# Kernel tuning notes

Hardware: AMD Instinct MI355X
Metric: run time of the kernel (lower is better)

The kernel has to match this reference:

```python
import jax, jax.numpy as jnp
import numpy as np

M, N, D = 4, 65536, 256

def setup_inputs() -> dict:
    key = jax.random.key(0)
    k1, k2, k3 = jax.random.split(key, 3)
    x = jax.random.normal(k1, (M, N, D), dtype=jnp.float32)
    # W[i,j] is the (out,in) weight of fusion_layers[i][j]; b[i,j] its bias.
    W = jax.random.normal(k2, (M, M, D, D), dtype=jnp.float32) * (1.0 / np.sqrt(D))
    b = jax.random.normal(k3, (M, M, D), dtype=jnp.float32) * 0.02
    return {"x": x, "W": W, "b": b}

def reference(x, W, b):
    # x: [M, N, D] stacked modality features (zip(*features) rows vectorized over N)
    # out[i] = x[i] + sum_{j != i} (x[j] @ W[i,j]^T + b[i,j])
    m = x.shape[0]
    mask = (1.0 - jnp.eye(m)).astype(x.dtype)            # zero on diagonal (skip i==j)
    y = jnp.einsum('ijef,jnf->ijne', W, x) + b[:, :, None, :]  # [M, M, N, D]
    out = x + jnp.einsum('ij,ijne->ine', mask, y)         # fused masked accumulation
    return out
```

## Files before the change

### kernel.cpp

```cpp
#include <hip/hip_runtime.h>
#include <hip/hip_bf16.h>
#include <stdint.h>

#define NN 65536
#define DD 256

typedef uint32_t u32;
typedef __attribute__((ext_vector_type(4))) float f32x4;
typedef __attribute__((ext_vector_type(4))) u32 u32x4;
typedef __attribute__((ext_vector_type(2))) u32 u32x2;
typedef __attribute__((ext_vector_type(8))) short s16x8;

__device__ inline unsigned short f2bf(float f) {
    union { float f; u32 u; } v; v.f = f;
    u32 u = v.u;
    return (unsigned short)((u + 0x7fffu + ((u >> 16) & 1u)) >> 16);
}

__device__ inline void gl2lds16(const void* g, void* s) {
    __builtin_amdgcn_global_load_lds(
        (const __attribute__((address_space(1))) void*)g,
        (__attribute__((address_space(3))) void*)s, 16, 0, 0);
}

__global__ void prep_w256(const float* __restrict__ W, unsigned short* __restrict__ Wimg) {
    int t = blockIdx.x * blockDim.x + threadIdx.x;
    int E = t * 4;
    int tile = E >> 14;
    int pin = E & 16383;
    int col = pin >> 6;
    int r2e = pin & 63;
    int ct = tile >> 4;
    int j = (tile >> 2) & 3;
    int kk = tile & 3;
    int kl = r2e ^ ((col & 7) << 3);
    int i = ct;
    int e = col;
    int f = kk * 64 + kl;
    u32 p0, p1;
    if (i == j) {
        unsigned short d0 = (e == f + 0) ? 0x3F80 : 0;
        unsigned short d1 = (e == f + 1) ? 0x3F80 : 0;
        unsigned short d2 = (e == f + 2) ? 0x3F80 : 0;
        unsigned short d3 = (e == f + 3) ? 0x3F80 : 0;
        p0 = (u32)d0 | ((u32)d1 << 16);
        p1 = (u32)d2 | ((u32)d3 << 16);
    } else {
        f32x4 w = *(const f32x4*)(W + ((size_t)((i * 4 + j) * 256 + e) << 8) + f);
        p0 = (u32)f2bf(w[0]) | ((u32)f2bf(w[1]) << 16);
        p1 = (u32)f2bf(w[2]) | ((u32)f2bf(w[3]) << 16);
    }
    u32x2 pr = {p0, p1};
    *(u32x2*)(Wimg + E) = pr;
}

__global__ void prep_w128(const float* __restrict__ W, unsigned short* __restrict__ Wimg) {
    int t = blockIdx.x * blockDim.x + threadIdx.x;
    int E = t * 4;
    int tile = E >> 13;
    int pin = E & 8191;
    int col = pin >> 6;
    int r2e = pin & 63;
    int ct = tile >> 4;
    int j = (tile >> 2) & 3;
    int kk = tile & 3;
    int kl = r2e ^ ((col & 7) << 3);
    int c = ct * 128 + col;
    int i = c >> 8, e = c & 255;
    int f = kk * 64 + kl;
    u32 p0, p1;
    if (i == j) {
        p0 = 0u; p1 = 0u;
    } else {
        f32x4 w = *(const f32x4*)(W + ((size_t)((i * 4 + j) * 256 + e) << 8) + f);
        p0 = (u32)f2bf(w[0]) | ((u32)f2bf(w[1]) << 16);
        p1 = (u32)f2bf(w[2]) | ((u32)f2bf(w[3]) << 16);
    }
    u32x2 pr = {p0, p1};
    *(u32x2*)(Wimg + E) = pr;
}

__global__ void prep_x(const float* __restrict__ x, unsigned short* __restrict__ Ximg) {
    int t = blockIdx.x * blockDim.x + threadIdx.x;
    long long E = (long long)t * 4;
    int tile = (int)(E >> 14);
    int pin = (int)(E & 16383);
    int row = pin >> 6;
    int r2e = pin & 63;
    int kk = tile & 3;
    int rt = (tile >> 2) & 255;
    int j = tile >> 10;
    int kl = r2e ^ ((row & 7) << 3);
    int n = rt * 256 + row;
    int f = kk * 64 + kl;
    f32x4 v = *(const f32x4*)(x + ((size_t)j * NN + n) * DD + f);
    u32 p0 = (u32)f2bf(v[0]) | ((u32)f2bf(v[1]) << 16);
    u32 p1 = (u32)f2bf(v[2]) | ((u32)f2bf(v[3]) << 16);
    u32x2 pr = {p0, p1};
    *(u32x2*)(Ximg + E) = pr;
}

__global__ void prep_b(const float* __restrict__ b, float* __restrict__ bsum) {
    int c = blockIdx.x * blockDim.x + threadIdx.x;
    if (c >= 1024) return;
    int i = c >> 8, e = c & 255;
    float s = 0.0f;
    #pragma unroll
    for (int j = 0; j < 4; ++j)
        if (j != i) s += b[((i * 4 + j) << 8) + e];
    bsum[c] = s;
}

__global__ __launch_bounds__(512, 2) void fusion_gemm4(
    const unsigned short* __restrict__ Wimg, const unsigned short* __restrict__ Ximg,
    const float* __restrict__ bsum, float* __restrict__ out) {
    __shared__ __attribute__((aligned(16))) char lds[2][65536];

    const int tid = threadIdx.x;
    const int bid = blockIdx.x;
    const int xcd = bid & 7;
    const int slot = bid >> 3;
    const int ct = slot & 3;
    const int rhi = slot >> 2;
    const int rtile = rhi * 8 + xcd;
    const int n0 = rtile * 256;
    const int col0 = ct * 256;

    const int lane = tid & 63;
    const int wid = tid >> 6;
    const int wm = wid & 1;
    const int wn = wid >> 1;

    f32x4 acc[8][4];
    #pragma unroll
    for (int a = 0; a < 8; ++a)
        #pragma unroll
        for (int b2 = 0; b2 < 4; ++b2)
            acc[a][b2] = (f32x4){0.f, 0.f, 0.f, 0.f};

    const char* WimgB = (const char*)Wimg;
    const char* XimgB = (const char*)Ximg;
    const u32 loff = (u32)(wid * 1024);
    const u32 goff = (u32)(wid * 1024 + lane * 16);

    s16x8 af[2][4];
    s16x8 bf2[2][2];

#define STAGE_PAIR(t_, q_)                                                            \
    {                                                                                 \
        int j_ = (t_) >> 2;                                                           \
        int kk_ = (t_) & 3;                                                           \
        const char* as_ = XimgB + (((size_t)((j_ * 256 + rtile) * 4 + kk_)) << 15)    \
                          + (q_) * 8192 + goff;                                       \
        gl2lds16(as_, ldsN + (q_) * 8192 + loff);                                     \
        const char* bs_ = WimgB + (((size_t)((ct * 4 + j_) * 4 + kk_)) << 15)         \
                          + (q_) * 8192 + goff;                                       \
        gl2lds16(bs_, ldsN + 32768 + (q_) * 8192 + loff);                             \
    }

#define RD_A(mh_)                                                                     \
    _Pragma("unroll")                                                                 \
    for (int kh = 0; kh < 2; ++kh) {                                                  \
        _Pragma("unroll")                                                             \
        for (int fm = 0; fm < 4; ++fm) {                                              \
            int r_ = wm * 128 + ((mh_) * 4 + fm) * 16 + (lane & 15);                  \
            u32 o_ = (u32)(r_ * 128 + kh * 64 + (lane >> 4) * 16);                    \
            o_ ^= (u32)((r_ & 7) << 4);                                               \
            af[kh][fm] = *(const s16x8*)(Ab + o_);                                    \
        }                                                                             \
    }

#define RD_B(nh_)                                                                     \
    _Pragma("unroll")                                                                 \
    for (int kh = 0; kh < 2; ++kh) {                                                  \
        _Pragma("unroll")                                                             \
        for (int fn = 0; fn < 2; ++fn) {                                              \
            int c_ = wn * 64 + ((nh_) * 2 + fn) * 16 + (lane & 15);                   \
            u32 o_ = (u32)(c_ * 128 + kh * 64 + (lane >> 4) * 16);                    \
            o_ ^= (u32)((c_ & 7) << 4);                                               \
            bf2[kh][fn] = *(const s16x8*)(Bb + o_);                                   \
        }                                                                             \
    }

#define MM_Q(mh_, nh_)                                                                \
    _Pragma("unroll")                                                                 \
    for (int kh = 0; kh < 2; ++kh) {                                                  \
        _Pragma("unroll")                                                             \
        for (int fm = 0; fm < 4; ++fm) {                                              \
            _Pragma("unroll")                                                         \
            for (int fn = 0; fn < 2; ++fn) {                                          \
                acc[(mh_) * 4 + fm][(nh_) * 2 + fn] =                                 \
                    __builtin_amdgcn_mfma_f32_16x16x32_bf16(                          \
                        af[kh][fm], bf2[kh][fn],                                      \
                        acc[(mh_) * 4 + fm][(nh_) * 2 + fn], 0, 0, 0);                \
            }                                                                         \
        }                                                                             \
    }

#define MFMA_CLUSTER(mh_, nh_)                                                        \
    __builtin_amdgcn_sched_barrier(0);                                                \
    __builtin_amdgcn_s_barrier();                                                     \
    __builtin_amdgcn_sched_barrier(0);                                                \
    __builtin_amdgcn_s_setprio(1);                                                    \
    MM_Q(mh_, nh_);                                                                   \
    __builtin_amdgcn_s_setprio(0);                                                    \
    __builtin_amdgcn_sched_barrier(0);                                                \
    __builtin_amdgcn_s_barrier();

    {
        char* ldsN = lds[0];
        STAGE_PAIR(0, 0);
        STAGE_PAIR(0, 1);
        STAGE_PAIR(0, 2);
        STAGE_PAIR(0, 3);
    }

    #pragma unroll 1
    for (int t = 0; t < 16; ++t) {
        const char* Ab = lds[t & 1];
        const char* Bb = Ab + 32768;
        char* ldsN = lds[(t + 1) & 1];

        if (t < 15) {
            STAGE_PAIR(t + 1, 0);
            asm volatile("s_waitcnt vmcnt(2)" ::: "memory");
        } else {
            asm volatile("s_waitcnt vmcnt(0)" ::: "memory");
        }
        __builtin_amdgcn_s_barrier();
        __builtin_amdgcn_sched_barrier(0);

        RD_A(0);
        RD_B(0);
        if (t < 15) STAGE_PAIR(t + 1, 1);
        MFMA_CLUSTER(0, 0);

        RD_B(1);
        if (t < 15) STAGE_PAIR(t + 1, 2);
        MFMA_CLUSTER(0, 1);

        RD_A(1);
        if (t < 15) STAGE_PAIR(t + 1, 3);
        MFMA_CLUSTER(1, 1);

        RD_B(0);
        MFMA_CLUSTER(1, 0);
    }

#undef STAGE_PAIR
#undef RD_A
#undef RD_B
#undef MM_Q
#undef MFMA_CLUSTER

    const int r0 = (lane >> 4) * 4;
    const int cl = lane & 15;
    #pragma unroll
    for (int mf = 0; mf < 8; ++mf) {
        #pragma unroll
        for (int nf = 0; nf < 4; ++nf) {
            int col_l = wn * 64 + nf * 16 + cl;
            float bs = bsum[col0 + col_l];
            #pragma unroll
            for (int r = 0; r < 4; ++r) {
                int n = n0 + wm * 128 + mf * 16 + r0 + r;
                size_t oidx = ((size_t)ct * NN + n) * DD + col_l;
                out[oidx] = acc[mf][nf][r] + bs;
            }
        }
    }
}

__global__ __launch_bounds__(256, 2) void fusion_gemm_fb(
    const float* __restrict__ x, const unsigned short* __restrict__ Wimg,
    const float* __restrict__ bsum, float* __restrict__ out) {
    __shared__ __attribute__((aligned(16))) unsigned short Alds[128 * 64];
    __shared__ __attribute__((aligned(16))) unsigned short Blds[2][128 * 64];

    const int tid = threadIdx.x;
    const int bid = blockIdx.x;
    const int xcd = bid & 7;
    const int slot = bid >> 3;
    const int ct = slot & 7;
    const int rhi = slot >> 3;
    const int rtile = rhi * 8 + xcd;
    const int n0 = rtile * 128;
    const int col0 = ct * 128;
    const int i = ct >> 1;

    const int lane = tid & 63;
    const int wid = tid >> 6;
    const int wm = wid >> 1;
    const int wn = wid & 1;

    f32x4 acc[4][4];
    #pragma unroll
    for (int a = 0; a < 4; ++a)
        #pragma unroll
        for (int b2 = 0; b2 < 4; ++b2)
            acc[a][b2] = (f32x4){0.f, 0.f, 0.f, 0.f};

    const int sr = tid >> 1;
    const int sh = tid & 1;
    char* Ab = (char*)Alds;
    const char* WimgB = (const char*)Wimg;

    f32x4 av[8];
    {
        int j0 = (i == 0) ? 1 : 0;
        const float* asrc = x + (size_t)j0 * ((size_t)NN * DD) + (size_t)(n0 + sr) * DD + sh * 32;
        #pragma unroll
        for (int q = 0; q < 8; ++q) av[q] = *(const f32x4*)(asrc + q * 4);
        const char* base = WimgB + (((size_t)(ct * 4 + j0) * 4 + 0) << 14) + wid * 1024 + lane * 16;
        char* lb = (char*)Blds[0] + wid * 1024;
        #pragma unroll
        for (int q = 0; q < 4; ++q) gl2lds16(base + q * 4096, lb + q * 4096);
    }

    for (int t = 0; t < 12; ++t) {
        __syncthreads();
        #pragma unroll
        for (int q = 0; q < 4; ++q) {
            f32x4 v0 = av[2 * q], v1 = av[2 * q + 1];
            u32x4 p;
            p[0] = (u32)f2bf(v0[0]) | ((u32)f2bf(v0[1]) << 16);
            p[1] = (u32)f2bf(v0[2]) | ((u32)f2bf(v0[3]) << 16);
            p[2] = (u32)f2bf(v1[0]) | ((u32)f2bf(v1[1]) << 16);
            p[3] = (u32)f2bf(v1[2]) | ((u32)f2bf(v1[3]) << 16);
            u32 o = (u32)(sr * 128 + sh * 64 + q * 16);
            o ^= (u32)((sr & 7) << 4);
            *(u32x4*)(Ab + o) = p;
        }
        __syncthreads();

        if (t < 11) {
            int tn = t + 1;
            int jjn = tn >> 2;
            int jn = jjn + (jjn >= i);
            int kkn = tn & 3;
            const char* base = WimgB + (((size_t)(ct * 4 + jn) * 4 + kkn) << 14) + wid * 1024 + lane * 16;
            char* lb = (char*)Blds[tn & 1] + wid * 1024;
            #pragma unroll
            for (int q = 0; q < 4; ++q) gl2lds16(base + q * 4096, lb + q * 4096);
            const float* asrc = x + (size_t)jn * ((size_t)NN * DD) + (size_t)(n0 + sr) * DD + kkn * 64 + sh * 32;
            #pragma unroll
            for (int q = 0; q < 8; ++q) av[q] = *(const f32x4*)(asrc + q * 4);
        }

        const char* Bb = (const char*)Blds[t & 1];
        #pragma unroll
        for (int kh = 0; kh < 2; ++kh) {
            s16x8 af[4], bfr[4];
            #pragma unroll
            for (int fm = 0; fm < 4; ++fm) {
                int row = wm * 64 + fm * 16 + (lane & 15);
                u32 o = (u32)(row * 128 + kh * 64 + (lane >> 4) * 16);
                o ^= (u32)((row & 7) << 4);
                af[fm] = *(const s16x8*)(Ab + o);
            }
            #pragma unroll
            for (int fn = 0; fn < 4; ++fn) {
                int col = wn * 64 + fn * 16 + (lane & 15);
                u32 o = (u32)(col * 128 + kh * 64 + (lane >> 4) * 16);
                o ^= (u32)((col & 7) << 4);
                bfr[fn] = *(const s16x8*)(Bb + o);
            }
            #pragma unroll
            for (int fm = 0; fm < 4; ++fm)
                #pragma unroll
                for (int fn = 0; fn < 4; ++fn)
                    acc[fm][fn] = __builtin_amdgcn_mfma_f32_16x16x32_bf16(
                        af[fm], bfr[fn], acc[fm][fn], 0, 0, 0);
        }
    }

    const int r0 = (lane >> 4) * 4;
    const int cl = lane & 15;
    #pragma unroll
    for (int fm = 0; fm < 4; ++fm) {
        #pragma unroll
        for (int fn = 0; fn < 4; ++fn) {
            int col_l = wn * 64 + fn * 16 + cl;
            int cglob = col0 + col_l;
            float bs = bsum[cglob];
            int e = cglob & 255;
            #pragma unroll
            for (int r = 0; r < 4; ++r) {
                int row_l = wm * 64 + fm * 16 + r0 + r;
                int n = n0 + row_l;
                size_t oidx = ((size_t)i * NN + n) * DD + e;
                out[oidx] = acc[fm][fn][r] + x[oidx] + bs;
            }
        }
    }
}

extern "C" void kernel_launch(void* const* d_in, const int* in_sizes, int n_in,
                              void* d_out, int out_size, void* d_ws, size_t ws_size,
                              hipStream_t stream) {
    const float* x = (const float*)d_in[0];
    const float* W = (const float*)d_in[1];
    const float* b = (const float*)d_in[2];
    float* out = (float*)d_out;

    unsigned short* Wimg = (unsigned short*)d_ws;
    float* bsum = (float*)((char*)d_ws + ((size_t)2 << 20));
    const size_t ximg_off = (size_t)4 << 20;
    const size_t need = ximg_off + ((size_t)128 << 20);

    hipLaunchKernelGGL(prep_b, dim3(4), dim3(256), 0, stream, b, bsum);

    if (ws_size >= need) {
        unsigned short* Ximg = (unsigned short*)((char*)d_ws + ximg_off);
        hipLaunchKernelGGL(prep_w256, dim3(1024), dim3(256), 0, stream, W, Wimg);
        hipLaunchKernelGGL(prep_x, dim3(65536), dim3(256), 0, stream, x, Ximg);
        hipLaunchKernelGGL(fusion_gemm4, dim3(1024), dim3(512), 0, stream, Wimg, Ximg, bsum, out);
    } else {
        hipLaunchKernelGGL(prep_w128, dim3(1024), dim3(256), 0, stream, W, Wimg);
        hipLaunchKernelGGL(fusion_gemm_fb, dim3(4096), dim3(256), 0, stream, x, Wimg, bsum, out);
    }
}
```

Before: 267.1 us.

## Software-pipeline LDS fragment reads across K-steps with double register sets

The GEMM main loop is restructured into a two-iteration unrolled schedule with separate register fragment sets (Aa/Ab, Bx/By/Bz). The next tile's first fragments are read from LDS during the current tile's last MFMA phase, and explicit lgkmcnt waits replace the barrier at the top of each iteration. This is meant to hide LDS read latency and global-to-LDS staging behind MFMA work. It raises register pressure and adds explicit vmcnt(0) waits. The workspace layout for bsum and Ximg is also shifted.

```diff
diff --git a/kernel.cpp b/kernel.cpp
--- a/kernel.cpp
+++ b/kernel.cpp
@@ -111,7 +111,7 @@
     bsum[c] = s;
 }
 
-__global__ __launch_bounds__(512, 2) void fusion_gemm4(
+__global__ __launch_bounds__(512, 2) void fusion_gemm5(
     const unsigned short* __restrict__ Wimg, const unsigned short* __restrict__ Ximg,
     const float* __restrict__ bsum, float* __restrict__ out) {
     __shared__ __attribute__((aligned(16))) char lds[2][65536];
@@ -143,22 +143,22 @@
     const u32 loff = (u32)(wid * 1024);
     const u32 goff = (u32)(wid * 1024 + lane * 16);
 
-    s16x8 af[2][4];
-    s16x8 bf2[2][2];
-
-#define STAGE_PAIR(t_, q_)                                                            \
+    s16x8 Aa[2][4], Ab[2][4];
+    s16x8 By[2][2], Bx[2][2], Bz[2][2];
+
+#define STG(t_, q_, D_)                                                               \
     {                                                                                 \
         int j_ = (t_) >> 2;                                                           \
         int kk_ = (t_) & 3;                                                           \
         const char* as_ = XimgB + (((size_t)((j_ * 256 + rtile) * 4 + kk_)) << 15)    \
                           + (q_) * 8192 + goff;                                       \
-        gl2lds16(as_, ldsN + (q_) * 8192 + loff);                                     \
+        gl2lds16(as_, (D_) + (q_) * 8192 + loff);                                     \
         const char* bs_ = WimgB + (((size_t)((ct * 4 + j_) * 4 + kk_)) << 15)         \
                           + (q_) * 8192 + goff;                                       \
-        gl2lds16(bs_, ldsN + 32768 + (q_) * 8192 + loff);                             \
-    }
-
-#define RD_A(mh_)                                                                     \
+        gl2lds16(bs_, (D_) + 32768 + (q_) * 8192 + loff);                             \
+    }
+
+#define RD_A(BUF_, mh_, SET_)                                                         \
     _Pragma("unroll")                                                                 \
     for (int kh = 0; kh < 2; ++kh) {                                                  \
         _Pragma("unroll")                                                             \
@@ -166,11 +166,11 @@
             int r_ = wm * 128 + ((mh_) * 4 + fm) * 16 + (lane & 15);                  \
             u32 o_ = (u32)(r_ * 128 + kh * 64 + (lane >> 4) * 16);                    \
             o_ ^= (u32)((r_ & 7) << 4);                                               \
-            af[kh][fm] = *(const s16x8*)(Ab + o_);                                    \
+            SET_[kh][fm] = *(const s16x8*)((BUF_) + o_);                              \
         }                                                                             \
     }
 
-#define RD_B(nh_)                                                                     \
+#define RD_B(BUF_, nh_, SET_)                                                         \
     _Pragma("unroll")                                                                 \
     for (int kh = 0; kh < 2; ++kh) {                                                  \
         _Pragma("unroll")                                                             \
@@ -178,11 +178,11 @@
             int c_ = wn * 64 + ((nh_) * 2 + fn) * 16 + (lane & 15);                   \
             u32 o_ = (u32)(c_ * 128 + kh * 64 + (lane >> 4) * 16);                    \
             o_ ^= (u32)((c_ & 7) << 4);                                               \
-            bf2[kh][fn] = *(const s16x8*)(Bb + o_);                                   \
+            SET_[kh][fn] = *(const s16x8*)((BUF_) + 32768 + o_);                      \
         }                                                                             \
     }
 
-#define MM_Q(mh_, nh_)                                                                \
+#define MM(AS_, BS_, mh_, nh_)                                                        \
     _Pragma("unroll")                                                                 \
     for (int kh = 0; kh < 2; ++kh) {                                                  \
         _Pragma("unroll")                                                             \
@@ -191,67 +191,75 @@
             for (int fn = 0; fn < 2; ++fn) {                                          \
                 acc[(mh_) * 4 + fm][(nh_) * 2 + fn] =                                 \
                     __builtin_amdgcn_mfma_f32_16x16x32_bf16(                          \
-                        af[kh][fm], bf2[kh][fn],                                      \
+                        AS_[kh][fm], BS_[kh][fn],                                     \
                         acc[(mh_) * 4 + fm][(nh_) * 2 + fn], 0, 0, 0);                \
             }                                                                         \
         }                                                                             \
     }
 
-#define MFMA_CLUSTER(mh_, nh_)                                                        \
-    __builtin_amdgcn_sched_barrier(0);                                                \
-    __builtin_amdgcn_s_barrier();                                                     \
-    __builtin_amdgcn_sched_barrier(0);                                                \
+#define SB __builtin_amdgcn_sched_barrier(0)
+#define BAR __builtin_amdgcn_s_barrier()
+#define LGKM(n_) asm volatile("s_waitcnt lgkmcnt(" #n_ ")" ::: "memory")
+#define VM0 asm volatile("s_waitcnt vmcnt(0)" ::: "memory")
+#define PHASE_MFMA(AS_, BS_, mh_, nh_, LG_)                                           \
+    SB; BAR; SB; LGKM(LG_); SB;                                                       \
     __builtin_amdgcn_s_setprio(1);                                                    \
-    MM_Q(mh_, nh_);                                                                   \
+    MM(AS_, BS_, mh_, nh_);                                                           \
     __builtin_amdgcn_s_setprio(0);                                                    \
-    __builtin_amdgcn_sched_barrier(0);                                                \
-    __builtin_amdgcn_s_barrier();
-
-    {
-        char* ldsN = lds[0];
-        STAGE_PAIR(0, 0);
-        STAGE_PAIR(0, 1);
-        STAGE_PAIR(0, 2);
-        STAGE_PAIR(0, 3);
-    }
+    SB; BAR;
+
+    char* Ebuf = lds[0];
+    char* Obuf = lds[1];
+
+    STG(0, 0, Ebuf); STG(0, 1, Ebuf); STG(0, 2, Ebuf); STG(0, 3, Ebuf);
+    VM0;
+    BAR; SB;
+    RD_A(Ebuf, 0, Aa);
+    RD_B(Ebuf, 0, Bx);
 
     #pragma unroll 1
-    for (int t = 0; t < 16; ++t) {
-        const char* Ab = lds[t & 1];
-        const char* Bb = Ab + 32768;
-        char* ldsN = lds[(t + 1) & 1];
-
-        if (t < 15) {
-            STAGE_PAIR(t + 1, 0);
-            asm volatile("s_waitcnt vmcnt(2)" ::: "memory");
+    for (int it = 0; it < 8; ++it) {
+        const int te = 2 * it;
+        const bool nl = (it < 7);
+
+        RD_B(Ebuf, 1, By);
+        STG(te + 1, 0, Obuf); STG(te + 1, 1, Obuf); STG(te + 1, 2, Obuf);
+        PHASE_MFMA(Aa, Bx, 0, 0, 4);
+        RD_A(Ebuf, 1, Ab);
+        STG(te + 1, 3, Obuf);
+        PHASE_MFMA(Aa, By, 0, 1, 8);
+        VM0;
+        PHASE_MFMA(Ab, By, 1, 1, 0);
+        RD_A(Obuf, 0, Aa);
+        RD_B(Obuf, 0, Bz);
+        PHASE_MFMA(Ab, Bx, 1, 0, 12);
+
+        RD_B(Obuf, 1, By);
+        if (nl) { STG(te + 2, 0, Ebuf); STG(te + 2, 1, Ebuf); STG(te + 2, 2, Ebuf); }
+        PHASE_MFMA(Aa, Bz, 0, 0, 4);
+        RD_A(Obuf, 1, Ab);
+        if (nl) STG(te + 2, 3, Ebuf);
+        PHASE_MFMA(Aa, By, 0, 1, 8);
+        VM0;
+        PHASE_MFMA(Ab, By, 1, 1, 0);
+        if (nl) {
+            RD_A(Ebuf, 0, Aa);
+            RD_B(Ebuf, 0, Bx);
+            PHASE_MFMA(Ab, Bz, 1, 0, 12);
         } else {
-            asm volatile("s_waitcnt vmcnt(0)" ::: "memory");
-        }
-        __builtin_amdgcn_s_barrier();
-        __builtin_amdgcn_sched_barrier(0);
-
-        RD_A(0);
-        RD_B(0);
-        if (t < 15) STAGE_PAIR(t + 1, 1);
-        MFMA_CLUSTER(0, 0);
-
-        RD_B(1);
-        if (t < 15) STAGE_PAIR(t + 1, 2);
-        MFMA_CLUSTER(0, 1);
-
-        RD_A(1);
-        if (t < 15) STAGE_PAIR(t + 1, 3);
-        MFMA_CLUSTER(1, 1);
-
-        RD_B(0);
-        MFMA_CLUSTER(1, 0);
-    }
-
-#undef STAGE_PAIR
+            PHASE_MFMA(Ab, Bz, 1, 0, 0);
+        }
+    }
+
+#undef STG
 #undef RD_A
 #undef RD_B
-#undef MM_Q
-#undef MFMA_CLUSTER
+#undef MM
+#undef SB
+#undef BAR
+#undef LGKM
+#undef VM0
+#undef PHASE_MFMA
 
     const int r0 = (lane >> 4) * 4;
     const int cl = lane & 15;
@@ -404,19 +412,21 @@
     float* out = (float*)d_out;
 
     unsigned short* Wimg = (unsigned short*)d_ws;
-    float* bsum = (float*)((char*)d_ws + ((size_t)2 << 20));
-    const size_t ximg_off = (size_t)4 << 20;
+    float* bsum = (float*)((char*)d_ws + ((size_t)8 << 20));
+    const size_t ximg_off = (size_t)9 << 20;
     const size_t need = ximg_off + ((size_t)128 << 20);
 
-    hipLaunchKernelGGL(prep_b, dim3(4), dim3(256), 0, stream, b, bsum);
-
     if (ws_size >= need) {
+        float* bsum2 = (float*)((char*)d_ws + ((size_t)8 << 20));
         unsigned short* Ximg = (unsigned short*)((char*)d_ws + ximg_off);
+        hipLaunchKernelGGL(prep_b, dim3(4), dim3(256), 0, stream, b, bsum2);
         hipLaunchKernelGGL(prep_w256, dim3(1024), dim3(256), 0, stream, W, Wimg);
         hipLaunchKernelGGL(prep_x, dim3(65536), dim3(256), 0, stream, x, Ximg);
-        hipLaunchKernelGGL(fusion_gemm4, dim3(1024), dim3(512), 0, stream, Wimg, Ximg, bsum, out);
+        hipLaunchKernelGGL(fusion_gemm5, dim3(1024), dim3(512), 0, stream, Wimg, Ximg, bsum2, out);
     } else {
+        float* bsum2 = (float*)((char*)d_ws + ((size_t)2 << 20));
+        hipLaunchKernelGGL(prep_b, dim3(4), dim3(256), 0, stream, b, bsum2);
         hipLaunchKernelGGL(prep_w128, dim3(1024), dim3(256), 0, stream, W, Wimg);
-        hipLaunchKernelGGL(fusion_gemm_fb, dim3(4096), dim3(256), 0, stream, x, Wimg, bsum, out);
-    }
-}
+        hipLaunchKernelGGL(fusion_gemm_fb, dim3(4096), dim3(256), 0, stream, x, Wimg, bsum2, out);
+    }
+}
```

Result: slower. 948.8 us (+255.2%).
